# Performance work log

Hardware: AMD Instinct MI355X
Metric: run time of the kernel (lower is better)

## Reference

```python
import jax, jax.numpy as jnp
import numpy as np

B, S, C, T = 16, 64, 20, 2048
_DIMS = [(20, 20), (20, 20), (20, 20), (20, 10), (10, 1)]


def setup_inputs() -> dict:
    key = jax.random.key(0)
    keys = jax.random.split(key, 1 + 2 * len(_DIMS))
    inp = {"data": jax.random.normal(keys[0], (B, S, C, T), dtype=jnp.float32)}
    for i, (din, dout) in enumerate(_DIMS):
        # weights stored (in, out); scaled like torch's default Linear init
        inp[f"W{i+1}"] = jax.random.normal(keys[1 + 2 * i], (din, dout), dtype=jnp.float32) / jnp.sqrt(jnp.float32(din))
        inp[f"b{i+1}"] = jax.random.normal(keys[2 + 2 * i], (dout,), dtype=jnp.float32) * 0.05
    return inp


def _mlp(x, Ws, bs):
    # x: (..., in_dim); five Linear+ReLU layers, final ReLU included
    h = x
    for W, b in zip(Ws, bs):
        h = jax.nn.relu(h @ W + b)
    return h


def reference(data, W1, b1, W2, b2, W3, b3, W4, b4, W5, b5):
    # data: (B, S, C, T) -> per-time-point features (B, S, T, C)
    x = jnp.swapaxes(data, 2, 3)
    y = _mlp(x, (W1, W2, W3, W4, W5), (b1, b2, b3, b4, b5))[..., 0]  # (B, S, T)
    t = y.shape[-1]
    yc = y - y.mean(axis=-1, keepdims=True)
    cov = jnp.einsum('bst,but->bsu', yc, yc) / jnp.float32(t - 1)  # (B, S, S)
    d = jnp.sqrt(jnp.diagonal(cov, axis1=1, axis2=2))  # (B, S)
    corr = cov / (d[:, :, None] * d[:, None, :])
    corr = jnp.clip(corr, -1.0, 1.0)  # torch.corrcoef clips real output
    return 1.0 - corr
```

## Files before the change

kernel.cpp:

```cpp
#include <hip/hip_runtime.h>

#define Bn 16
#define Sn 64
#define Cn 20
#define Tn 2048
#define TPB 256
#define KS 8
#define Kc (Tn / KS)
#define PITCH 260

template <int NJ>
__device__ __forceinline__ void layer2(const float (&in)[2][20], float (&out)[2][20],
                                       const float* __restrict__ WT,
                                       const float* __restrict__ bb) {
    #pragma unroll
    for (int j = 0; j < NJ; ++j) {
        float a0 = bb[j], a1 = bb[j];
        const float4* wr = (const float4*)(WT + j * 20);
        #pragma unroll
        for (int q = 0; q < 5; ++q) {
            const float4 w = wr[q];
            a0 = fmaf(in[0][4 * q + 0], w.x, a0);  a1 = fmaf(in[1][4 * q + 0], w.x, a1);
            a0 = fmaf(in[0][4 * q + 1], w.y, a0);  a1 = fmaf(in[1][4 * q + 1], w.y, a1);
            a0 = fmaf(in[0][4 * q + 2], w.z, a0);  a1 = fmaf(in[1][4 * q + 2], w.z, a1);
            a0 = fmaf(in[0][4 * q + 3], w.w, a0);  a1 = fmaf(in[1][4 * q + 3], w.w, a1);
        }
        out[0][j] = fmaxf(a0, 0.f);
        out[1][j] = fmaxf(a1, 0.f);
    }
}

__global__ __launch_bounds__(256) void mlp_kernel(
    const float* __restrict__ data,
    const float* __restrict__ W1, const float* __restrict__ b1,
    const float* __restrict__ W2, const float* __restrict__ b2,
    const float* __restrict__ W3, const float* __restrict__ b3,
    const float* __restrict__ W4, const float* __restrict__ b4,
    const float* __restrict__ W5, const float* __restrict__ b5,
    float* __restrict__ y, double* __restrict__ Rp)
{
    __shared__ __align__(16) float sW1T[400], sW2T[400], sW3T[400], sW4T[200];
    __shared__ float sW5[10], sb1[20], sb2[20], sb3[20], sb4[10], sb5v[1];
    __shared__ double rbuf[TPB];

    const int tid = threadIdx.x;
    for (int i = tid; i < 400; i += TPB) {
        const int j = i / 20, c = i % 20;
        sW1T[i] = W1[c * 20 + j];
        sW2T[i] = W2[c * 20 + j];
        sW3T[i] = W3[c * 20 + j];
    }
    if (tid < 200) { const int j = tid / 20, c = tid % 20; sW4T[tid] = W4[c * 10 + j]; }
    if (tid < 20) { sb1[tid] = b1[tid]; sb2[tid] = b2[tid]; sb3[tid] = b3[tid]; }
    if (tid < 10) { sW5[tid] = W5[tid]; sb4[tid] = b4[tid]; }
    if (tid == 0) sb5v[0] = b5[0];
    __syncthreads();

    const int bs = blockIdx.x >> 2;
    const int qt = blockIdx.x & 3;
    const float* base = data + (size_t)bs * Cn * Tn;
    const int t0 = qt * (Tn / 4) + tid * 2;

    float x[2][20], h[2][20];
    #pragma unroll
    for (int c = 0; c < 20; ++c) {
        const float2 v = *(const float2*)&base[c * Tn + t0];
        x[0][c] = v.x; x[1][c] = v.y;
    }

    layer2<20>(x, h, sW1T, sb1);
    layer2<20>(h, x, sW2T, sb2);
    layer2<20>(x, h, sW3T, sb3);
    layer2<10>(h, x, sW4T, sb4);

    float yv[2];
    #pragma unroll
    for (int m = 0; m < 2; ++m) {
        float yy = sb5v[0];
        #pragma unroll
        for (int i = 0; i < 10; ++i) yy = fmaf(x[m][i], sW5[i], yy);
        yv[m] = fmaxf(yy, 0.f);
    }
    float2 st; st.x = yv[0]; st.y = yv[1];
    *(float2*)&y[(size_t)bs * Tn + t0] = st;

    rbuf[tid] = (double)yv[0] + (double)yv[1];
    __syncthreads();
    for (int off = 128; off > 0; off >>= 1) {
        if (tid < off) rbuf[tid] += rbuf[tid + off];
        __syncthreads();
    }
    if (tid == 0) Rp[blockIdx.x] = rbuf[0];
}

__global__ __launch_bounds__(256) void cov_kernel(
    const float* __restrict__ y, const double* __restrict__ Rp,
    float* __restrict__ covf)
{
    __shared__ __align__(16) float S[64 * PITCH];
    __shared__ double smean[64];

    const int tid = threadIdx.x;
    const int b  = blockIdx.x >> 3;
    const int ks = blockIdx.x & 7;

    if (tid < 64) {
        const int q = ((b << 6) + tid) * 4;
        smean[tid] = (Rp[q] + Rp[q + 1] + Rp[q + 2] + Rp[q + 3]) * (1.0 / Tn);
    }
    __syncthreads();

    const float* ybase = y + (size_t)(b << 6) * Tn + ks * Kc;
    #pragma unroll
    for (int it = 0; it < (64 * Kc / 4) / TPB; ++it) {
        const int f4 = tid + it * TPB;
        const int row = f4 >> 6;
        const int k4 = f4 & 63;
        const float4 v = *(const float4*)&ybase[(size_t)row * Tn + k4 * 4];
        const double m = smean[row];
        float4 c;
        c.x = (float)((double)v.x - m);
        c.y = (float)((double)v.y - m);
        c.z = (float)((double)v.z - m);
        c.w = (float)((double)v.w - m);
        *(float4*)&S[row * PITCH + k4 * 4] = c;
    }
    __syncthreads();

    const int ty = tid >> 4, tx = tid & 15;
    float acc[4][4];
    #pragma unroll
    for (int a = 0; a < 4; ++a)
        #pragma unroll
        for (int j = 0; j < 4; ++j) acc[a][j] = 0.f;

    for (int kq = 0; kq < Kc / 4; ++kq) {
        float4 av[4], bv[4];
        #pragma unroll
        for (int a = 0; a < 4; ++a) av[a] = *(const float4*)&S[(ty + 16 * a) * PITCH + kq * 4];
        #pragma unroll
        for (int j = 0; j < 4; ++j) bv[j] = *(const float4*)&S[(tx + 16 * j) * PITCH + kq * 4];
        #pragma unroll
        for (int a = 0; a < 4; ++a)
            #pragma unroll
            for (int j = 0; j < 4; ++j) {
                acc[a][j] = fmaf(av[a].x, bv[j].x, acc[a][j]);
                acc[a][j] = fmaf(av[a].y, bv[j].y, acc[a][j]);
                acc[a][j] = fmaf(av[a].z, bv[j].z, acc[a][j]);
                acc[a][j] = fmaf(av[a].w, bv[j].w, acc[a][j]);
            }
    }

    float* cb = covf + ((size_t)b << 12);
    #pragma unroll
    for (int a = 0; a < 4; ++a) {
        const int row = ty + 16 * a;
        #pragma unroll
        for (int j = 0; j < 4; ++j)
            atomicAdd(&cb[(row << 6) + tx + 16 * j], acc[a][j]);
    }
}

__global__ __launch_bounds__(256) void corr_kernel(
    const float* __restrict__ covf, float* __restrict__ out)
{
    const int i = blockIdx.x * TPB + threadIdx.x;
    if (i >= Bn * Sn * Sn) return;
    const int b = i / (Sn * Sn);
    const int rem = i % (Sn * Sn);
    const int s = rem / Sn, u = rem % Sn;
    const double css = (double)covf[((size_t)b * Sn + s) * Sn + s];
    const double cuu = (double)covf[((size_t)b * Sn + u) * Sn + u];
    const double csu = (double)covf[i];
    double r = csu / sqrt(css * cuu);
    r = (r < -1.0) ? -1.0 : ((r > 1.0) ? 1.0 : r);
    out[i] = (float)(1.0 - r);
}

extern "C" void kernel_launch(void* const* d_in, const int* in_sizes, int n_in,
                              void* d_out, int out_size, void* d_ws, size_t ws_size,
                              hipStream_t stream) {
    const float* data = (const float*)d_in[0];
    const float* W1 = (const float*)d_in[1];  const float* b1 = (const float*)d_in[2];
    const float* W2 = (const float*)d_in[3];  const float* b2 = (const float*)d_in[4];
    const float* W3 = (const float*)d_in[5];  const float* b3 = (const float*)d_in[6];
    const float* W4 = (const float*)d_in[7];  const float* b4 = (const float*)d_in[8];
    const float* W5 = (const float*)d_in[9];  const float* b5 = (const float*)d_in[10];
    float* out = (float*)d_out;

    float* y = (float*)d_ws;
    float* covf = (float*)((char*)d_ws + (size_t)Bn * Sn * Tn * sizeof(float));
    double* Rp = (double*)((char*)covf + (size_t)Bn * Sn * Sn * sizeof(float));

    hipMemsetAsync(covf, 0, (size_t)Bn * Sn * Sn * sizeof(float), stream);
    mlp_kernel<<<Bn * Sn * 4, TPB, 0, stream>>>(data, W1, b1, W2, b2, W3, b3, W4, b4, W5, b5, y, Rp);
    cov_kernel<<<Bn * KS, TPB, 0, stream>>>(y, Rp, covf);
    corr_kernel<<<(Bn * Sn * Sn + TPB - 1) / TPB, TPB, 0, stream>>>(covf, out);
}
```

Baseline: 304.9 us.

## Read MLP weights from global, use wave-shuffle reduction, split covariance K wider

The MLP kernel no longer stages transposed weights in shared memory. It reads weights directly from global memory, where uniform indices should become scalar loads, and uses an input-outer, output-inner FMA order. This drops the per-block weight staging and its barrier. The block sum reduction now uses 64-wide wave shuffles instead of an 8-step shared-memory tree. The covariance kernel splits T into 32 chunks instead of 8, giving 512 blocks for better occupancy, at the cost of four times as many atomic adds into the covariance buffer.

```diff
diff --git a/kernel.cpp b/kernel.cpp
--- a/kernel.cpp
+++ b/kernel.cpp
@@ -5,28 +5,35 @@
 #define Cn 20
 #define Tn 2048
 #define TPB 256
-#define KS 8
+#define KS 32
 #define Kc (Tn / KS)
-#define PITCH 260
+#define PITCH 68
 
-template <int NJ>
-__device__ __forceinline__ void layer2(const float (&in)[2][20], float (&out)[2][20],
-                                       const float* __restrict__ WT,
-                                       const float* __restrict__ bb) {
+template <int NI, int NJ>
+__device__ __forceinline__ void layerS(const float (&in)[2][NI], float (&out)[2][NJ],
+                                       const float* __restrict__ W,
+                                       const float* __restrict__ bb)
+{
+    float acc[2][NJ];
     #pragma unroll
     for (int j = 0; j < NJ; ++j) {
-        float a0 = bb[j], a1 = bb[j];
-        const float4* wr = (const float4*)(WT + j * 20);
+        const float bj = bb[j];
+        acc[0][j] = bj; acc[1][j] = bj;
+    }
+    #pragma unroll
+    for (int c = 0; c < NI; ++c) {
+        const float x0 = in[0][c], x1 = in[1][c];
         #pragma unroll
-        for (int q = 0; q < 5; ++q) {
-            const float4 w = wr[q];
-            a0 = fmaf(in[0][4 * q + 0], w.x, a0);  a1 = fmaf(in[1][4 * q + 0], w.x, a1);
-            a0 = fmaf(in[0][4 * q + 1], w.y, a0);  a1 = fmaf(in[1][4 * q + 1], w.y, a1);
-            a0 = fmaf(in[0][4 * q + 2], w.z, a0);  a1 = fmaf(in[1][4 * q + 2], w.z, a1);
-            a0 = fmaf(in[0][4 * q + 3], w.w, a0);  a1 = fmaf(in[1][4 * q + 3], w.w, a1);
+        for (int j = 0; j < NJ; ++j) {
+            const float w = W[c * NJ + j];
+            acc[0][j] = fmaf(x0, w, acc[0][j]);
+            acc[1][j] = fmaf(x1, w, acc[1][j]);
         }
-        out[0][j] = fmaxf(a0, 0.f);
-        out[1][j] = fmaxf(a1, 0.f);
+    }
+    #pragma unroll
+    for (int j = 0; j < NJ; ++j) {
+        out[0][j] = fmaxf(acc[0][j], 0.f);
+        out[1][j] = fmaxf(acc[1][j], 0.f);
     }
 }
 
@@ -39,23 +46,9 @@
     const float* __restrict__ W5, const float* __restrict__ b5,
     float* __restrict__ y, double* __restrict__ Rp)
 {
-    __shared__ __align__(16) float sW1T[400], sW2T[400], sW3T[400], sW4T[200];
-    __shared__ float sW5[10], sb1[20], sb2[20], sb3[20], sb4[10], sb5v[1];
-    __shared__ double rbuf[TPB];
+    __shared__ double rbuf[TPB / 64];
 
     const int tid = threadIdx.x;
-    for (int i = tid; i < 400; i += TPB) {
-        const int j = i / 20, c = i % 20;
-        sW1T[i] = W1[c * 20 + j];
-        sW2T[i] = W2[c * 20 + j];
-        sW3T[i] = W3[c * 20 + j];
-    }
-    if (tid < 200) { const int j = tid / 20, c = tid % 20; sW4T[tid] = W4[c * 10 + j]; }
-    if (tid < 20) { sb1[tid] = b1[tid]; sb2[tid] = b2[tid]; sb3[tid] = b3[tid]; }
-    if (tid < 10) { sW5[tid] = W5[tid]; sb4[tid] = b4[tid]; }
-    if (tid == 0) sb5v[0] = b5[0];
-    __syncthreads();
-
     const int bs = blockIdx.x >> 2;
     const int qt = blockIdx.x & 3;
     const float* base = data + (size_t)bs * Cn * Tn;
@@ -68,29 +61,23 @@
         x[0][c] = v.x; x[1][c] = v.y;
     }
 
-    layer2<20>(x, h, sW1T, sb1);
-    layer2<20>(h, x, sW2T, sb2);
-    layer2<20>(x, h, sW3T, sb3);
-    layer2<10>(h, x, sW4T, sb4);
+    layerS<20, 20>(x, h, W1, b1);
+    layerS<20, 20>(h, x, W2, b2);
+    layerS<20, 20>(x, h, W3, b3);
+    float g[2][10];
+    layerS<20, 10>(h, g, W4, b4);
+    float o[2][1];
+    layerS<10, 1>(g, o, W5, b5);
 
-    float yv[2];
-    #pragma unroll
-    for (int m = 0; m < 2; ++m) {
-        float yy = sb5v[0];
-        #pragma unroll
-        for (int i = 0; i < 10; ++i) yy = fmaf(x[m][i], sW5[i], yy);
-        yv[m] = fmaxf(yy, 0.f);
-    }
-    float2 st; st.x = yv[0]; st.y = yv[1];
+    float2 st; st.x = o[0][0]; st.y = o[1][0];
     *(float2*)&y[(size_t)bs * Tn + t0] = st;
 
-    rbuf[tid] = (double)yv[0] + (double)yv[1];
+    double r = (double)o[0][0] + (double)o[1][0];
+    #pragma unroll
+    for (int off = 32; off > 0; off >>= 1) r += __shfl_down(r, off, 64);
+    if ((tid & 63) == 0) rbuf[tid >> 6] = r;
     __syncthreads();
-    for (int off = 128; off > 0; off >>= 1) {
-        if (tid < off) rbuf[tid] += rbuf[tid + off];
-        __syncthreads();
-    }
-    if (tid == 0) Rp[blockIdx.x] = rbuf[0];
+    if (tid == 0) Rp[blockIdx.x] = rbuf[0] + rbuf[1] + rbuf[2] + rbuf[3];
 }
 
 __global__ __launch_bounds__(256) void cov_kernel(
@@ -101,8 +88,8 @@
     __shared__ double smean[64];
 
     const int tid = threadIdx.x;
-    const int b  = blockIdx.x >> 3;
-    const int ks = blockIdx.x & 7;
+    const int b  = blockIdx.x >> 5;
+    const int ks = blockIdx.x & 31;
 
     if (tid < 64) {
         const int q = ((b << 6) + tid) * 4;
@@ -114,8 +101,8 @@
     #pragma unroll
     for (int it = 0; it < (64 * Kc / 4) / TPB; ++it) {
         const int f4 = tid + it * TPB;
-        const int row = f4 >> 6;
-        const int k4 = f4 & 63;
+        const int row = f4 >> 4;
+        const int k4 = f4 & 15;
         const float4 v = *(const float4*)&ybase[(size_t)row * Tn + k4 * 4];
         const double m = smean[row];
         float4 c;
```

New measurement: 307.3 us. No clear change (+0.8%).
